# Optimization experiments

Measured on AMD Instinct MI355X. Metric: run time of the kernel, lower is better.

## Reference

```python
import jax, jax.numpy as jnp
import numpy as np

B, L, H = 4, 96, 512
R, T = 257, 21


def setup_inputs() -> dict:
    key = jax.random.key(0)
    ks = jax.random.split(key, 7)
    std_in = (2.0 / (H + 1 + R)) ** 0.5  # xavier_normal over [H+1, R]
    return {
        "layer1": jax.random.normal(ks[0], (B, L, H), jnp.float32),
        "layer2": jax.random.normal(ks[1], (B, L, H), jnp.float32),
        "layer3": jax.random.normal(ks[2], (B, L, H), jnp.float32),
        "W_1": jax.random.normal(ks[3], (H + 1, R), jnp.float32) * std_in,
        "W_2": jax.random.normal(ks[4], (H + 1, R), jnp.float32) * std_in,
        "W_3": jax.random.normal(ks[5], (H + 1, R), jnp.float32) * std_in,
        "W_l": jax.random.normal(ks[6], (1, R, T), jnp.float32),
    }


def reference(layer1, layer2, layer3, W_1, W_2, W_3, W_l):
    # Append bias-ones feature, as in the torch forward.
    ones = jnp.ones((*layer1.shape[:2], 1), layer1.dtype)
    l1 = jnp.concatenate([layer1, ones], axis=-1)  # [n, i, H+1]
    l2 = jnp.concatenate([layer2, ones], axis=-1)  # [n, j, H+1]
    l3 = jnp.concatenate([layer3, jnp.ones((*layer3.shape[:-1], 1), layer3.dtype)], axis=-1)
    # Factor the CP contraction: project each stream to rank space first.
    p1 = jnp.einsum("nia,ar->nir", l1, W_1)  # [n, i, r]
    p2 = jnp.einsum("njb,br->njr", l2, W_2)  # [n, j, r]
    p3 = jnp.einsum("nkc,cr->nkr", l3, W_3)  # [n, k, r]
    # Fold label map into one stream, then rank-reduce outer product.
    p3t = jnp.einsum("nkr,rt->ntkr", p3, W_l[0])  # [n, t, k, r]
    out = jnp.einsum("nir,njr,ntkr->ntijk", p1, p2, p3t)  # [n, t, i, j, k]
    return out
```

## Files before the change

### kernel.cpp

```cpp
#include <hip/hip_runtime.h>
#include <hip/hip_bf16.h>

#define RR 257
#define RP 288
#define TT 21

typedef __attribute__((ext_vector_type(4))) float f32x4;
typedef __attribute__((ext_vector_type(8))) short bf16x8;

union Pack8 { unsigned short s[8]; uint4 v; };

__device__ __forceinline__ unsigned short f2b(float f) {
    union { float f; unsigned u; } v; v.f = f;
    unsigned r = v.u + 0x7fffu + ((v.u >> 16) & 1u);
    return (unsigned short)(r >> 16);
}

__global__ __launch_bounds__(384) void proj_kernel(
    const float* __restrict__ l1, const float* __restrict__ l2, const float* __restrict__ l3,
    const float* __restrict__ W1, const float* __restrict__ W2, const float* __restrict__ W3,
    float* __restrict__ P1f, float* __restrict__ P2f, float* __restrict__ P3f)
{
    int bx = blockIdx.x;
    int grp = bx % 24;
    int n = (bx / 24) & 3;
    int s = bx / 96;
    const float* layer = (s == 0) ? l1 : (s == 1) ? l2 : l3;
    const float* W     = (s == 0) ? W1 : (s == 1) ? W2 : W3;
    int i0 = grp * 4;

    __shared__ __attribute__((aligned(16))) float x[2048];
    const float4* src = (const float4*)(layer + (n * 96 + i0) * 512);
    float4* xv = (float4*)x;
    for (int idx = threadIdx.x; idx < 512; idx += 384) xv[idx] = src[idx];
    __syncthreads();

    int r = threadIdx.x;
    if (r < RP) {
        float a0 = 0.f, a1 = 0.f, a2 = 0.f, a3 = 0.f;
        if (r < RR) {
            float b = W[512 * RR + r];
            a0 = a1 = a2 = a3 = b;
            #pragma unroll 8
            for (int a = 0; a < 512; ++a) {
                float wa = W[a * RR + r];
                a0 = fmaf(x[a], wa, a0);
                a1 = fmaf(x[512 + a], wa, a1);
                a2 = fmaf(x[1024 + a], wa, a2);
                a3 = fmaf(x[1536 + a], wa, a3);
            }
        }
        float* P = (s == 0) ? P1f : (s == 1) ? P2f : P3f;
        int base = (n * 96 + i0) * RP + r;
        P[base]          = a0;
        P[base + RP]     = a1;
        P[base + 2 * RP] = a2;
        P[base + 3 * RP] = a3;
    }
}

__global__ __launch_bounds__(256) void aprep_kernel(
    const float* __restrict__ P1f, const float* __restrict__ P2f,
    unsigned short* __restrict__ Af)
{
    int bx = blockIdx.x;
    int n = bx / 96, i = bx % 96;
    __shared__ __attribute__((aligned(16))) float p1row[RP];
    for (int r = threadIdx.x; r < RP; r += 256)
        p1row[r] = P1f[(n * 96 + i) * RP + r];
    __syncthreads();

    unsigned short* dst = Af + (size_t)(n * 576 + i * 6) * 9 * 512;
    for (int idx = threadIdx.x; idx < 3456; idx += 256) {
        int L = idx & 63;
        int rest = idx >> 6;
        int ks = rest % 9, rgl = rest / 9;
        int j = rgl * 16 + (L & 15);
        int k8 = ks * 32 + (L >> 4) * 8;
        const float* p2p = P2f + (n * 96 + j) * RP + k8;
        float4 b0 = *(const float4*)(p2p);
        float4 b1 = *(const float4*)(p2p + 4);
        float4 a0 = *(const float4*)(p1row + k8);
        float4 a1 = *(const float4*)(p1row + k8 + 4);
        Pack8 u;
        u.s[0] = f2b(a0.x * b0.x); u.s[1] = f2b(a0.y * b0.y);
        u.s[2] = f2b(a0.z * b0.z); u.s[3] = f2b(a0.w * b0.w);
        u.s[4] = f2b(a1.x * b1.x); u.s[5] = f2b(a1.y * b1.y);
        u.s[6] = f2b(a1.z * b1.z); u.s[7] = f2b(a1.w * b1.w);
        *(uint4*)(dst + (size_t)(rgl * 9 + ks) * 512 + L * 8) = u.v;
    }
}

__global__ __launch_bounds__(256) void bprep_kernel(
    const float* __restrict__ P3f, const float* __restrict__ Wl,
    unsigned short* __restrict__ Bf)
{
    int bx = blockIdx.x;
    int t = bx % TT, n = bx / TT;
    __shared__ __attribute__((aligned(16))) float wl_lds[RP];
    for (int r = threadIdx.x; r < RP; r += 256)
        wl_lds[r] = (r < RR) ? Wl[r * TT + t] : 0.f;
    __syncthreads();

    unsigned short* dst = Bf + (size_t)(n * TT + t) * 6 * 9 * 512;
    for (int idx = threadIdx.x; idx < 3456; idx += 256) {
        int L = idx & 63;
        int rest = idx >> 6;
        int ks = rest % 9, kg = rest / 9;
        int col = kg * 16 + (L & 15);
        int r8 = ks * 32 + (L >> 4) * 8;
        const float* p3p = P3f + (n * 96 + col) * RP + r8;
        float4 p0 = *(const float4*)(p3p);
        float4 p1 = *(const float4*)(p3p + 4);
        float4 w0 = *(const float4*)(wl_lds + r8);
        float4 w1 = *(const float4*)(wl_lds + r8 + 4);
        Pack8 u;
        u.s[0] = f2b(p0.x * w0.x); u.s[1] = f2b(p0.y * w0.y);
        u.s[2] = f2b(p0.z * w0.z); u.s[3] = f2b(p0.w * w0.w);
        u.s[4] = f2b(p1.x * w1.x); u.s[5] = f2b(p1.y * w1.y);
        u.s[6] = f2b(p1.z * w1.z); u.s[7] = f2b(p1.w * w1.w);
        *(uint4*)(dst + (size_t)(kg * 9 + ks) * 512 + L * 8) = u.v;
    }
}

__global__ __launch_bounds__(512, 4) void tri5_kernel(
    const unsigned short* __restrict__ Af, const unsigned short* __restrict__ Bf,
    float* __restrict__ out)
{
    int orig = blockIdx.x;
    int bx = (orig & 7) * 378 + (orig >> 3);
    int t = bx % TT;
    int mtn = bx / TT;
    int mt = mtn % 36;
    int n = mtn / 36;

    int tid = threadIdx.x, lane = tid & 63, wv = tid >> 6;

    __shared__ __attribute__((aligned(16))) unsigned short blds[27648];

    {
        const uint4* bsrc = (const uint4*)(Bf + (size_t)(n * TT + t) * 27648);
        uint4* bdst = (uint4*)blds;
        for (int idx = tid; idx < 3456; idx += 512) bdst[idx] = bsrc[idx];
    }
    __syncthreads();

    const unsigned short* abase =
        Af + (size_t)(n * 576 + mt * 16 + wv * 2) * 9 * 512 + lane * 8;
    const unsigned short* lbase = blds + lane * 8;

    f32x4 acc[2][6] = {};
    bf16x8 fa[2][2], fb[6];

    fa[0][0] = *(const bf16x8*)(abase + 0 * 512);
    fa[0][1] = *(const bf16x8*)(abase + 9 * 512);

    #pragma unroll
    for (int ks = 0; ks < 9; ++ks) {
        int cur = ks & 1, nxt = cur ^ 1;
        if (ks < 8) {
            fa[nxt][0] = *(const bf16x8*)(abase + (0 * 9 + ks + 1) * 512);
            fa[nxt][1] = *(const bf16x8*)(abase + (1 * 9 + ks + 1) * 512);
        }
        #pragma unroll
        for (int nf = 0; nf < 6; ++nf)
            fb[nf] = *(const bf16x8*)(lbase + (nf * 9 + ks) * 512);
        __builtin_amdgcn_s_setprio(1);
        #pragma unroll
        for (int mf = 0; mf < 2; ++mf)
            #pragma unroll
            for (int nf = 0; nf < 6; ++nf)
                acc[mf][nf] = __builtin_amdgcn_mfma_f32_16x16x32_bf16(
                    fb[nf], fa[cur][mf], acc[mf][nf], 0, 0, 0);
        __builtin_amdgcn_s_setprio(0);
    }

    __syncthreads();
    float* tb = (float*)blds + wv * 1600;
    int Llo = lane & 15, Lhi = lane >> 4;
    size_t outbase = ((size_t)(n * TT + t) * 9216 + mt * 256 + wv * 32) * 96;

    #pragma unroll
    for (int mf = 0; mf < 2; ++mf) {
        #pragma unroll
        for (int nf = 0; nf < 6; ++nf)
            *(f32x4*)&tb[Llo * 100 + nf * 16 + Lhi * 4] = acc[mf][nf];
        float* gdst = out + outbase + (size_t)mf * 16 * 96;
        #pragma unroll
        for (int q = 0; q < 6; ++q) {
            int fidx = q * 64 + lane;
            int ml = fidx / 24, k4 = fidx % 24;
            f32x4 vv = *(const f32x4*)&tb[ml * 100 + k4 * 4];
            __builtin_nontemporal_store(vv, (f32x4*)(gdst + (size_t)fidx * 4));
        }
    }
}

extern "C" void kernel_launch(void* const* d_in, const int* in_sizes, int n_in,
                              void* d_out, int out_size, void* d_ws, size_t ws_size,
                              hipStream_t stream) {
    const float* l1 = (const float*)d_in[0];
    const float* l2 = (const float*)d_in[1];
    const float* l3 = (const float*)d_in[2];
    const float* W1 = (const float*)d_in[3];
    const float* W2 = (const float*)d_in[4];
    const float* W3 = (const float*)d_in[5];
    const float* Wl = (const float*)d_in[6];

    float* P1f = (float*)d_ws;
    float* P2f = P1f + 384 * RP;
    float* P3f = P2f + 384 * RP;
    unsigned short* Af = (unsigned short*)(P3f + 384 * RP);
    unsigned short* Bf = Af + (size_t)4 * 576 * 9 * 512;

    proj_kernel<<<288, 384, 0, stream>>>(l1, l2, l3, W1, W2, W3, P1f, P2f, P3f);
    aprep_kernel<<<384, 256, 0, stream>>>(P1f, P2f, Af);
    bprep_kernel<<<84, 256, 0, stream>>>(P3f, Wl, Bf);
    tri5_kernel<<<3024, 512, 0, stream>>>(Af, Bf, (float*)d_out);
}
```

Measured before the change: 121.1 us.

## Enlarge per-wave output tile to 6x6 MFMA fragments, halve block size

```diff
diff --git a/kernel.cpp b/kernel.cpp
--- a/kernel.cpp
+++ b/kernel.cpp
@@ -96,14 +96,16 @@
     unsigned short* __restrict__ Bf)
 {
     int bx = blockIdx.x;
-    int t = bx % TT, n = bx / TT;
+    int h = bx & 1;
+    int t = (bx >> 1) % TT, n = bx / (2 * TT);
     __shared__ __attribute__((aligned(16))) float wl_lds[RP];
     for (int r = threadIdx.x; r < RP; r += 256)
         wl_lds[r] = (r < RR) ? Wl[r * TT + t] : 0.f;
     __syncthreads();
 
     unsigned short* dst = Bf + (size_t)(n * TT + t) * 6 * 9 * 512;
-    for (int idx = threadIdx.x; idx < 3456; idx += 256) {
+    for (int idx2 = threadIdx.x; idx2 < 1728; idx2 += 256) {
+        int idx = h * 1728 + idx2;
         int L = idx & 63;
         int rest = idx >> 6;
         int ks = rest % 9, kg = rest / 9;
@@ -123,16 +125,24 @@
     }
 }
 
-__global__ __launch_bounds__(512, 4) void tri5_kernel(
+#define LOADA(s, kss) { _Pragma("unroll") for (int mf = 0; mf < 6; ++mf) \
+    fa[s][mf] = *(const bf16x8*)(abase + (mf * 9 + (kss)) * 512); }
+#define LOADB(kss) { _Pragma("unroll") for (int nf = 0; nf < 6; ++nf) \
+    fb[nf] = *(const bf16x8*)(lbase + (nf * 9 + (kss)) * 512); }
+#define MFMAS(s) { _Pragma("unroll") for (int nf = 0; nf < 6; ++nf) { \
+    _Pragma("unroll") for (int mf = 0; mf < 6; ++mf) \
+      acc[mf][nf] = __builtin_amdgcn_mfma_f32_16x16x32_bf16(fb[nf], fa[s][mf], acc[mf][nf], 0, 0, 0); } }
+
+__global__ __launch_bounds__(256, 2) void tri8_kernel(
     const unsigned short* __restrict__ Af, const unsigned short* __restrict__ Bf,
     float* __restrict__ out)
 {
     int orig = blockIdx.x;
-    int bx = (orig & 7) * 378 + (orig >> 3);
+    int bx = (orig & 7) * 252 + (orig >> 3);
     int t = bx % TT;
     int mtn = bx / TT;
-    int mt = mtn % 36;
-    int n = mtn / 36;
+    int mt = mtn % 24;
+    int n = mtn / 24;
 
     int tid = threadIdx.x, lane = tid & 63, wv = tid >> 6;
 
@@ -141,47 +151,34 @@
     {
         const uint4* bsrc = (const uint4*)(Bf + (size_t)(n * TT + t) * 27648);
         uint4* bdst = (uint4*)blds;
-        for (int idx = tid; idx < 3456; idx += 512) bdst[idx] = bsrc[idx];
+        for (int idx = tid; idx < 3456; idx += 256) bdst[idx] = bsrc[idx];
     }
     __syncthreads();
 
     const unsigned short* abase =
-        Af + (size_t)(n * 576 + mt * 16 + wv * 2) * 9 * 512 + lane * 8;
+        Af + (size_t)(n * 576 + mt * 24 + wv * 6) * 9 * 512 + lane * 8;
     const unsigned short* lbase = blds + lane * 8;
 
-    f32x4 acc[2][6] = {};
-    bf16x8 fa[2][2], fb[6];
-
-    fa[0][0] = *(const bf16x8*)(abase + 0 * 512);
-    fa[0][1] = *(const bf16x8*)(abase + 9 * 512);
-
+    f32x4 acc[6][6] = {};
+    bf16x8 fa[2][6], fb[6];
+
+    LOADA(0, 0);
     #pragma unroll
     for (int ks = 0; ks < 9; ++ks) {
-        int cur = ks & 1, nxt = cur ^ 1;
         if (ks < 8) {
-            fa[nxt][0] = *(const bf16x8*)(abase + (0 * 9 + ks + 1) * 512);
-            fa[nxt][1] = *(const bf16x8*)(abase + (1 * 9 + ks + 1) * 512);
+            if (ks & 1) { LOADA(0, ks + 1); } else { LOADA(1, ks + 1); }
         }
-        #pragma unroll
-        for (int nf = 0; nf < 6; ++nf)
-            fb[nf] = *(const bf16x8*)(lbase + (nf * 9 + ks) * 512);
-        __builtin_amdgcn_s_setprio(1);
-        #pragma unroll
-        for (int mf = 0; mf < 2; ++mf)
-            #pragma unroll
-            for (int nf = 0; nf < 6; ++nf)
-                acc[mf][nf] = __builtin_amdgcn_mfma_f32_16x16x32_bf16(
-                    fb[nf], fa[cur][mf], acc[mf][nf], 0, 0, 0);
-        __builtin_amdgcn_s_setprio(0);
+        LOADB(ks);
+        if (ks & 1) { MFMAS(1); } else { MFMAS(0); }
     }
 
     __syncthreads();
     float* tb = (float*)blds + wv * 1600;
     int Llo = lane & 15, Lhi = lane >> 4;
-    size_t outbase = ((size_t)(n * TT + t) * 9216 + mt * 256 + wv * 32) * 96;
+    size_t outbase = ((size_t)(n * TT + t) * 9216 + mt * 384 + wv * 96) * 96;
 
     #pragma unroll
-    for (int mf = 0; mf < 2; ++mf) {
+    for (int mf = 0; mf < 6; ++mf) {
         #pragma unroll
         for (int nf = 0; nf < 6; ++nf)
             *(f32x4*)&tb[Llo * 100 + nf * 16 + Lhi * 4] = acc[mf][nf];
@@ -215,6 +212,6 @@
 
     proj_kernel<<<288, 384, 0, stream>>>(l1, l2, l3, W1, W2, W3, P1f, P2f, P3f);
     aprep_kernel<<<384, 256, 0, stream>>>(P1f, P2f, Af);
-    bprep_kernel<<<84, 256, 0, stream>>>(P3f, Wl, Bf);
-    tri5_kernel<<<3024, 512, 0, stream>>>(Af, Bf, (float*)d_out);
-}
+    bprep_kernel<<<168, 256, 0, stream>>>(P3f, Wl, Bf);
+    tri8_kernel<<<2016, 256, 0, stream>>>(Af, Bf, (float*)d_out);
+}
```

Result: faster. 116.4 us (-3.9%).
